# Kernel optimization log

Measured on AMD Instinct MI355X. Metric: run time of the kernel, lower is better.

Reference implementation:

```python
import jax, jax.numpy as jnp
import numpy as np

B, L, D, H = 4, 1024, 1024, 16
E = 16384
HD = D // H  # head dim = 64


def setup_inputs() -> dict:
    key = jax.random.key(0)
    k1, k2, k3, k4 = jax.random.split(key, 4)
    x = jax.random.normal(k1, (B, L, D), dtype=jnp.float32)
    edges = jax.random.randint(k2, (E, 2), 0, L, dtype=jnp.int32)
    w_qkv = jax.random.normal(k3, (3 * D, D), dtype=jnp.float32) * 0.02
    b_qkv = jnp.zeros((3 * D,), dtype=jnp.float32)
    w_out = jax.random.normal(k4, (D, D), dtype=jnp.float32) * 0.02
    b_out = jnp.zeros((D,), dtype=jnp.float32)
    return {"x": x, "edges": edges, "w_qkv": w_qkv, "b_qkv": b_qkv,
            "w_out": w_out, "b_out": b_out}


def reference(x, edges, w_qkv, b_qkv, w_out, b_out):
    # Build symmetric boolean adjacency mask [L, L]; True = edge present.
    adj = jnp.zeros((L, L), dtype=bool)
    adj = adj.at[edges[:, 0], edges[:, 1]].set(True)
    adj = adj.at[edges[:, 1], edges[:, 0]].set(True)

    # Fused QKV projection (torch MultiheadAttention in_proj).
    qkv = x @ w_qkv.T + b_qkv                      # [B, L, 3D]
    q, k, v = jnp.split(qkv, 3, axis=-1)           # each [B, L, D]

    def heads(t):  # [B, L, D] -> [B, H, L, HD]
        return t.reshape(B, L, H, HD).transpose(0, 2, 1, 3)

    q, k, v = heads(q), heads(k), heads(v)
    scale = 1.0 / np.sqrt(HD)
    scores = jnp.einsum('bhqd,bhkd->bhqk', q * scale, k)  # [B, H, L, L]
    # torch bool attn_mask: True means NOT allowed to attend -> -inf.
    scores = jnp.where(adj[None, None, :, :], -jnp.inf, scores)
    attn = jax.nn.softmax(scores, axis=-1)
    out = jnp.einsum('bhqk,bhkd->bhqd', attn, v)   # [B, H, L, HD]
    out = out.transpose(0, 2, 1, 3).reshape(B, L, D)
    return out @ w_out.T + b_out
```

## Files before the change

### kernel.cpp

```cpp
#include <hip/hip_runtime.h>
#include <hip/hip_bf16.h>
#include <stdint.h>

#define B_   4
#define L_   1024
#define D_   1024
#define H_   16
#define HD_  64
#define E_   16384
#define BH_  (B_*H_)
#define BL_  (B_*L_)

typedef __bf16 bf16;
typedef __bf16 bf16x8 __attribute__((ext_vector_type(8)));
typedef float  f32x4  __attribute__((ext_vector_type(4)));

#if __has_builtin(__builtin_amdgcn_exp2f)
#define EXP2F(x) __builtin_amdgcn_exp2f(x)
#else
#define EXP2F(x) exp2f(x)
#endif

#define QSCALE 0.18033688011112042f

__device__ __forceinline__ void gload_lds16(const bf16* gsrc, bf16* lds_dst) {
  __builtin_amdgcn_global_load_lds(
      (const __attribute__((address_space(1))) unsigned int*)gsrc,
      (__attribute__((address_space(3))) unsigned int*)lds_dst,
      16, 0, 0);
}

__global__ void k_detect(const unsigned short* __restrict__ w,
                         unsigned int* __restrict__ flag) {
  int i = blockIdx.x * 256 + threadIdx.x;
  unsigned short u = w[i];
  int e = (u >> 7) & 0xFF;
  if (e >= 200) atomicOr(flag, 1u);
}

__global__ __launch_bounds__(256) void k_castall(
    const void* __restrict__ x, const void* __restrict__ wq,
    const void* __restrict__ wo, const void* __restrict__ bq,
    const void* __restrict__ bo,
    bf16* __restrict__ xb, bf16* __restrict__ wqb, bf16* __restrict__ wob,
    float* __restrict__ bqf, float* __restrict__ bof,
    const unsigned int* __restrict__ flag) {
  const long e = ((long)blockIdx.x * 256 + threadIdx.x) * 8;
  const bool f = *flag != 0;
  const long N0 = 4l << 20, N1 = N0 + (3l << 20), N2 = N1 + (1l << 20);
  const void* src;
  bf16* d16 = nullptr; float* d32 = nullptr; long j;
  if (e < N0)      { src = x;  d16 = xb;  j = e; }
  else if (e < N1) { src = wq; d16 = wqb; j = e - N0; }
  else if (e < N2) { src = wo; d16 = wob; j = e - N1; }
  else {
    long b = e - N2;
    if (b < 3072)      { src = bq; d32 = bqf; j = b; }
    else if (b < 4096) { src = bo; d32 = bof; j = b - 3072; }
    else return;
  }
  if (d16) {
    bf16x8 v;
    if (f) {
      const float* s = (const float*)src + j;
#pragma unroll
      for (int q = 0; q < 8; ++q) v[q] = (bf16)s[q];
    } else {
      v = *(const bf16x8*)((const bf16*)src + j);
    }
    *(bf16x8*)(d16 + j) = v;
  } else {
    if (f) {
      const f32x4* s = (const f32x4*)((const float*)src + j);
      f32x4 a = s[0], b2 = s[1];
      *(f32x4*)(d32 + j) = a;
      *((f32x4*)(d32 + j) + 1) = b2;
    } else {
      const bf16* s = (const bf16*)src + j;
#pragma unroll
      for (int q = 0; q < 8; ++q) d32[j + q] = (float)s[q];
    }
  }
}

__global__ void k_adj(const int* __restrict__ edges,
                      unsigned long long* __restrict__ adj) {
  int i = blockIdx.x * 256 + threadIdx.x;
  if (i < E_) {
    int a = edges[2 * i], b = edges[2 * i + 1];
    atomicOr(&adj[a * 16 + (b >> 6)], 1ull << (b & 63));
    atomicOr(&adj[b * 16 + (a >> 6)], 1ull << (a & 63));
  }
}

template <bool QKV>
__global__ __launch_bounds__(256) void k_gemm(
    const bf16* __restrict__ A, const bf16* __restrict__ W,
    const float* __restrict__ bias, void* __restrict__ outv,
    const unsigned int* __restrict__ flag,
    bf16* __restrict__ qb, bf16* __restrict__ kb, bf16* __restrict__ vb) {
  constexpr int K = 1024;
  __shared__ __align__(16) bf16 As[128 * 32];
  __shared__ __align__(16) bf16 Bs[128 * 32];

  const int t = threadIdx.x;
  const int lane = t & 63, w = t >> 6;
  const int wm = w >> 1, wn = w & 1;
  const int quad = lane >> 4, l16 = lane & 15;
  const int m0 = blockIdx.y * 128, n0 = blockIdx.x * 128;

  const bf16* Abase = A + m0 * K;
  const bf16* Wbase = W + n0 * K;

  f32x4 acc[4][4] = {};

  for (int kt = 0; kt < K; kt += 32) {
#pragma unroll
    for (int j = 0; j < 2; ++j) {
      int o = (j * 256 + t) * 16;
      int row = o >> 6;
      int col = (o & 63) >> 1;
      gload_lds16(Abase + row * K + kt + col, &As[(j * 256 + w * 64) * 8]);
      gload_lds16(Wbase + row * K + kt + col, &Bs[(j * 256 + w * 64) * 8]);
    }
    asm volatile("s_waitcnt vmcnt(0)" ::: "memory");
    __syncthreads();

    bf16x8 af[4], bfv[4];
#pragma unroll
    for (int i = 0; i < 4; ++i) {
      af[i]  = *(const bf16x8*)&As[(wm * 64 + i * 16 + l16) * 32 + quad * 8];
      bfv[i] = *(const bf16x8*)&Bs[(wn * 64 + i * 16 + l16) * 32 + quad * 8];
    }
#pragma unroll
    for (int mi = 0; mi < 4; ++mi)
#pragma unroll
      for (int ni = 0; ni < 4; ++ni)
        acc[mi][ni] = __builtin_amdgcn_mfma_f32_16x16x32_bf16(
            af[mi], bfv[ni], acc[mi][ni], 0, 0, 0);
    __syncthreads();
  }

#pragma unroll
  for (int ni = 0; ni < 4; ++ni) {
    int col = n0 + wn * 64 + ni * 16 + l16;
    float bv = bias[col];
    if constexpr (QKV) {
      int which = col >> 10;
      int hcol = col & 1023;
      int h = hcol >> 6, hd = hcol & 63;
#pragma unroll
      for (int mi = 0; mi < 4; ++mi)
#pragma unroll
        for (int r = 0; r < 4; ++r) {
          int row = m0 + wm * 64 + mi * 16 + quad * 4 + r;
          int bb = row >> 10, l = row & 1023;
          int bh = bb * H_ + h;
          float v = acc[mi][ni][r] + bv;
          if (which == 0)      qb[(bh * L_ + l) * HD_ + hd] = (bf16)(v * QSCALE);
      else if (which == 1)     kb[(bh * L_ + l) * HD_ + hd] = (bf16)v;
      else                     vb[(bh * HD_ + hd) * L_ + l] = (bf16)v;
        }
    } else {
      bool f32out = (*flag != 0);
#pragma unroll
      for (int mi = 0; mi < 4; ++mi)
#pragma unroll
        for (int r = 0; r < 4; ++r) {
          int row = m0 + wm * 64 + mi * 16 + quad * 4 + r;
          float v = acc[mi][ni][r] + bv;
          if (f32out) ((float*)outv)[row * 1024 + col] = v;
          else        ((bf16*)outv)[row * 1024 + col] = (bf16)v;
        }
    }
  }
}

__global__ __launch_bounds__(256, 4) void k_attn(
    const bf16* __restrict__ qb, const bf16* __restrict__ kb,
    const bf16* __restrict__ vb, const unsigned long long* __restrict__ adj,
    bf16* __restrict__ aout) {
  __shared__ __align__(16) bf16 Ks[2 * 64 * 64];
  __shared__ __align__(16) bf16 Vt[2 * 64 * 64];
  __shared__ __align__(16) bf16 Ps[64 * 64];

  const int t = threadIdx.x, lane = t & 63, w = t >> 6;
  const int quad = lane >> 4, l16 = lane & 15;
  const int bh = blockIdx.y, qt = blockIdx.x;
  const int q0 = qt * 64 + w * 16;

  const bf16* qbase = qb + (size_t)bh * (L_ * HD_);
  const bf16* kbase = kb + (size_t)bh * (L_ * HD_);
  const bf16* vbase = vb + (size_t)bh * (HD_ * L_);

  bf16x8 aq[2];
#pragma unroll
  for (int c = 0; c < 2; ++c)
    aq[c] = *(const bf16x8*)&qbase[(q0 + l16) * HD_ + c * 32 + quad * 8];

  const int vr = lane >> 3;
  const int scol = ((lane & 7) ^ vr) * 8;
  const bf16* ksrc0 = kbase + (w * 16 + vr) * HD_ + scol;
  const bf16* ksrc1 = kbase + (w * 16 + 8 + vr) * HD_ + scol;
  const bf16* vsrc0 = vbase + (w * 16 + vr) * L_ + scol;
  const bf16* vsrc1 = vbase + (w * 16 + 8 + vr) * L_ + scol;

  const unsigned long long* adjrow = adj + (size_t)(q0 + quad * 4) * 16;

  float l_acc[4] = {0.f, 0.f, 0.f, 0.f};
  f32x4 o_acc[4] = {};

  const int psoff = (quad * 16) ^ ((l16 & 7) << 4);
  const int pswrow = (w * 16 + quad * 4) * 64;

#define STAGE_KV(i1) do {                                          \
    const int bo_ = ((i1) & 1) * 4096;                             \
    gload_lds16(ksrc0 + (i1) * 4096, &Ks[bo_ + (w * 16) * 64]);     \
    gload_lds16(ksrc1 + (i1) * 4096, &Ks[bo_ + (w * 16 + 8) * 64]); \
    gload_lds16(vsrc0 + (i1) * 64,   &Vt[bo_ + (w * 16) * 64]);     \
    gload_lds16(vsrc1 + (i1) * 64,   &Vt[bo_ + (w * 16 + 8) * 64]); \
  } while (0)

  STAGE_KV(0);

#pragma unroll 1
  for (int i = 0; i < 16; ++i) {
    const int bufo = (i & 1) * 4096;

    unsigned long long wmask[4];
#pragma unroll
    for (int r = 0; r < 4; ++r) wmask[r] = adjrow[r * 16 + i];

    if (i < 15) STAGE_KV(i + 1);

    if (i < 15) asm volatile("s_waitcnt vmcnt(8)" ::: "memory");
    else        asm volatile("s_waitcnt vmcnt(4)" ::: "memory");
    __builtin_amdgcn_s_barrier();

    f32x4 s[4];
#pragma unroll
    for (int nt = 0; nt < 4; ++nt) {
      f32x4 z = {};
#pragma unroll
      for (int c = 0; c < 2; ++c) {
        bf16x8 bk = *(const bf16x8*)&Ks[bufo + (nt * 16 + l16) * 64 +
            ((psoff ^ (c << 6)) >> 1)];
        z = __builtin_amdgcn_mfma_f32_16x16x32_bf16(aq[c], bk, z, 0, 0, 0);
      }
      s[nt] = z;
    }

#pragma unroll
    for (int r = 0; r < 4; ++r) {
      unsigned long long wr = wmask[r] >> l16;
      float pr = 0.f;
#pragma unroll
      for (int nt = 0; nt < 4; ++nt) {
        float sv = s[nt][r];
        if ((wr >> (nt * 16)) & 1ull) sv = -60000.f;
        float p = EXP2F(sv);
        int colb = (nt * 32 + l16 * 2) ^ (((quad * 4 + r) & 7) << 4);
        Ps[pswrow + r * 64 + (colb >> 1)] = (bf16)p;
        pr += p;
      }
      l_acc[r] += pr;
    }

#pragma unroll
    for (int c = 0; c < 2; ++c) {
      bf16x8 ap = *(const bf16x8*)
          &Ps[(w * 16 + l16) * 64 + ((psoff ^ (c << 6)) >> 1)];
#pragma unroll
      for (int nt = 0; nt < 4; ++nt) {
        bf16x8 bv = *(const bf16x8*)
            &Vt[bufo + (nt * 16 + l16) * 64 + ((psoff ^ (c << 6)) >> 1)];
        o_acc[nt] = __builtin_amdgcn_mfma_f32_16x16x32_bf16(ap, bv, o_acc[nt], 0, 0, 0);
      }
    }
    __builtin_amdgcn_s_barrier();
  }
#undef STAGE_KV

#pragma unroll
  for (int x = 1; x < 16; x <<= 1)
#pragma unroll
    for (int r = 0; r < 4; ++r)
      l_acc[r] += __shfl_xor(l_acc[r], x, 64);

  const int bb = bh >> 4, h = bh & 15;
#pragma unroll
  for (int r = 0; r < 4; ++r) {
    const float inv = l_acc[r] > 0.f ? 1.f / l_acc[r] : 0.f;
    const int qrow = q0 + quad * 4 + r;
    bf16* orow = aout + ((size_t)(bb * L_ + qrow)) * D_ + h * HD_;
#pragma unroll
    for (int nt = 0; nt < 4; ++nt)
      orow[nt * 16 + l16] = (bf16)(o_acc[nt][r] * inv);
  }
}

extern "C" void kernel_launch(void* const* d_in, const int* in_sizes, int n_in,
                              void* d_out, int out_size, void* d_ws, size_t ws_size,
                              hipStream_t stream) {
  const void* x_raw  = d_in[0];
  const int*  edges  = (const int*)d_in[1];
  const void* wq_raw = d_in[2];
  const void* bq_raw = d_in[3];
  const void* wo_raw = d_in[4];
  const void* bo_raw = d_in[5];

  char* ws = (char*)d_ws;
  unsigned int*        flag = (unsigned int*)ws;
  unsigned long long*  adj  = (unsigned long long*)(ws + 1024);
  size_t off = 1024 + 131072;
  bf16* xb    = (bf16*)(ws + off); off += (size_t)BL_ * D_ * 2;
  bf16* wqkvb = (bf16*)(ws + off); off += (size_t)3 * D_ * D_ * 2;
  bf16* woutb = (bf16*)(ws + off); off += (size_t)D_ * D_ * 2;
  float* bqf  = (float*)(ws + off); off += 3 * D_ * 4;
  float* bof  = (float*)(ws + off); off += D_ * 4;
  bf16* qb    = (bf16*)(ws + off); off += (size_t)BH_ * L_ * HD_ * 2;
  bf16* kb    = (bf16*)(ws + off); off += (size_t)BH_ * L_ * HD_ * 2;
  bf16* vb    = (bf16*)(ws + off); off += (size_t)BH_ * L_ * HD_ * 2;
  bf16* abuf  = (bf16*)(ws + off);

  hipMemsetAsync(ws, 0, 1024 + 131072, stream);
  k_detect<<<dim3(512), dim3(256), 0, stream>>>(
      (const unsigned short*)wq_raw, flag);

  k_castall<<<dim3(4098), dim3(256), 0, stream>>>(
      x_raw, wq_raw, wo_raw, bq_raw, bo_raw,
      xb, wqkvb, woutb, bqf, bof, flag);

  k_adj<<<dim3(E_ / 256), dim3(256), 0, stream>>>(edges, adj);

  k_gemm<true><<<dim3(24, 32), dim3(256), 0, stream>>>(
      xb, wqkvb, bqf, nullptr, flag, qb, kb, vb);
  k_attn<<<dim3(16, 64), dim3(256), 0, stream>>>(qb, kb, vb, adj, abuf);
  k_gemm<false><<<dim3(8, 32), dim3(256), 0, stream>>>(
      abuf, woutb, bof, d_out, flag, nullptr, nullptr, nullptr);
}
```

Before: 217.1 us.

## Double-buffer GEMM LDS loads with XOR swizzle and fuse detect/adjacency into cast

The GEMM main loop now keeps two LDS buffers and issues the next K-tile's global-to-LDS loads before computing the current one, waiting with a partial vmcnt. This overlaps memory latency with MFMA work. LDS columns are XOR-swizzled by row to reduce bank conflicts on fragment reads. The dtype-detection and adjacency-building kernels are folded into the cast kernel, which removes two launches. Each block now rereads a small slice of the weight to decide the dtype locally, and the LDS footprint doubles.

```diff
diff --git a/kernel.cpp b/kernel.cpp
--- a/kernel.cpp
+++ b/kernel.cpp
@@ -14,6 +14,7 @@
 typedef __bf16 bf16;
 typedef __bf16 bf16x8 __attribute__((ext_vector_type(8)));
 typedef float  f32x4  __attribute__((ext_vector_type(4)));
+typedef unsigned short u16x8 __attribute__((ext_vector_type(8)));
 
 #if __has_builtin(__builtin_amdgcn_exp2f)
 #define EXP2F(x) __builtin_amdgcn_exp2f(x)
@@ -30,23 +31,33 @@
       16, 0, 0);
 }
 
-__global__ void k_detect(const unsigned short* __restrict__ w,
-                         unsigned int* __restrict__ flag) {
-  int i = blockIdx.x * 256 + threadIdx.x;
-  unsigned short u = w[i];
-  int e = (u >> 7) & 0xFF;
-  if (e >= 200) atomicOr(flag, 1u);
-}
-
 __global__ __launch_bounds__(256) void k_castall(
     const void* __restrict__ x, const void* __restrict__ wq,
     const void* __restrict__ wo, const void* __restrict__ bq,
     const void* __restrict__ bo,
+    const int* __restrict__ edges, unsigned long long* __restrict__ adj,
     bf16* __restrict__ xb, bf16* __restrict__ wqb, bf16* __restrict__ wob,
     float* __restrict__ bqf, float* __restrict__ bof,
-    const unsigned int* __restrict__ flag) {
-  const long e = ((long)blockIdx.x * 256 + threadIdx.x) * 8;
-  const bool f = *flag != 0;
+    unsigned int* __restrict__ flag_out) {
+  const int t = threadIdx.x;
+
+  bool lf = false;
+  {
+    u16x8 u = *(const u16x8*)((const unsigned short*)wq + (size_t)t * 8);
+#pragma unroll
+    for (int q = 0; q < 8; ++q) lf |= (((u[q] >> 7) & 0xFF) >= 200);
+  }
+  const bool f = __any(lf);
+  if (blockIdx.x == 0 && t == 0 && f) *flag_out = 1u;
+
+  if (blockIdx.x < 64) {
+    int i = blockIdx.x * 256 + t;
+    int a = edges[2 * i], b = edges[2 * i + 1];
+    atomicOr(&adj[a * 16 + (b >> 6)], 1ull << (b & 63));
+    atomicOr(&adj[b * 16 + (a >> 6)], 1ull << (a & 63));
+  }
+
+  const long e = ((long)blockIdx.x * 256 + t) * 8;
   const long N0 = 4l << 20, N1 = N0 + (3l << 20), N2 = N1 + (1l << 20);
   const void* src;
   bf16* d16 = nullptr; float* d32 = nullptr; long j;
@@ -83,16 +94,6 @@
   }
 }
 
-__global__ void k_adj(const int* __restrict__ edges,
-                      unsigned long long* __restrict__ adj) {
-  int i = blockIdx.x * 256 + threadIdx.x;
-  if (i < E_) {
-    int a = edges[2 * i], b = edges[2 * i + 1];
-    atomicOr(&adj[a * 16 + (b >> 6)], 1ull << (b & 63));
-    atomicOr(&adj[b * 16 + (a >> 6)], 1ull << (a & 63));
-  }
-}
-
 template <bool QKV>
 __global__ __launch_bounds__(256) void k_gemm(
     const bf16* __restrict__ A, const bf16* __restrict__ W,
@@ -100,8 +101,8 @@
     const unsigned int* __restrict__ flag,
     bf16* __restrict__ qb, bf16* __restrict__ kb, bf16* __restrict__ vb) {
   constexpr int K = 1024;
-  __shared__ __align__(16) bf16 As[128 * 32];
-  __shared__ __align__(16) bf16 Bs[128 * 32];
+  __shared__ __align__(16) bf16 As[2 * 128 * 32];
+  __shared__ __align__(16) bf16 Bs[2 * 128 * 32];
 
   const int t = threadIdx.x;
   const int lane = t & 63, w = t >> 6;
@@ -112,25 +113,43 @@
   const bf16* Abase = A + m0 * K;
   const bf16* Wbase = W + n0 * K;
 
+  const int srow = t >> 2;
+  const int scolb = (t & 3) << 4;
+  const int scol = (scolb ^ ((srow & 3) << 4)) >> 1;
+  const bf16* asrc0 = Abase + srow * K + scol;
+  const bf16* asrc1 = Abase + (srow + 64) * K + scol;
+  const bf16* wsrc0 = Wbase + srow * K + scol;
+  const bf16* wsrc1 = Wbase + (srow + 64) * K + scol;
+
+  const int fo = ((quad * 16) ^ ((l16 & 3) << 4)) >> 1;
+
   f32x4 acc[4][4] = {};
 
-  for (int kt = 0; kt < K; kt += 32) {
-#pragma unroll
-    for (int j = 0; j < 2; ++j) {
-      int o = (j * 256 + t) * 16;
-      int row = o >> 6;
-      int col = (o & 63) >> 1;
-      gload_lds16(Abase + row * K + kt + col, &As[(j * 256 + w * 64) * 8]);
-      gload_lds16(Wbase + row * K + kt + col, &Bs[(j * 256 + w * 64) * 8]);
-    }
-    asm volatile("s_waitcnt vmcnt(0)" ::: "memory");
-    __syncthreads();
+#define STAGE_AB(it1) do {                                          \
+    const int bo_ = ((it1) & 1) * 4096;                              \
+    gload_lds16(asrc0 + (it1) * 32, &As[bo_ + (w * 64) * 8]);        \
+    gload_lds16(asrc1 + (it1) * 32, &As[bo_ + (256 + w * 64) * 8]);  \
+    gload_lds16(wsrc0 + (it1) * 32, &Bs[bo_ + (w * 64) * 8]);        \
+    gload_lds16(wsrc1 + (it1) * 32, &Bs[bo_ + (256 + w * 64) * 8]);  \
+  } while (0)
+
+  STAGE_AB(0);
+
+#pragma unroll 1
+  for (int it = 0; it < 32; ++it) {
+    const int bo = (it & 1) * 4096;
+
+    if (it < 31) STAGE_AB(it + 1);
+
+    if (it < 31) asm volatile("s_waitcnt vmcnt(4)" ::: "memory");
+    else         asm volatile("s_waitcnt vmcnt(0)" ::: "memory");
+    __builtin_amdgcn_s_barrier();
 
     bf16x8 af[4], bfv[4];
 #pragma unroll
     for (int i = 0; i < 4; ++i) {
-      af[i]  = *(const bf16x8*)&As[(wm * 64 + i * 16 + l16) * 32 + quad * 8];
-      bfv[i] = *(const bf16x8*)&Bs[(wn * 64 + i * 16 + l16) * 32 + quad * 8];
+      af[i]  = *(const bf16x8*)&As[bo + (wm * 64 + i * 16 + l16) * 32 + fo];
+      bfv[i] = *(const bf16x8*)&Bs[bo + (wn * 64 + i * 16 + l16) * 32 + fo];
     }
 #pragma unroll
     for (int mi = 0; mi < 4; ++mi)
@@ -138,8 +157,9 @@
       for (int ni = 0; ni < 4; ++ni)
         acc[mi][ni] = __builtin_amdgcn_mfma_f32_16x16x32_bf16(
             af[mi], bfv[ni], acc[mi][ni], 0, 0, 0);
-    __syncthreads();
-  }
+    __builtin_amdgcn_s_barrier();
+  }
+#undef STAGE_AB
 
 #pragma unroll
   for (int ni = 0; ni < 4; ++ni) {
@@ -324,14 +344,10 @@
   bf16* abuf  = (bf16*)(ws + off);
 
   hipMemsetAsync(ws, 0, 1024 + 131072, stream);
-  k_detect<<<dim3(512), dim3(256), 0, stream>>>(
-      (const unsigned short*)wq_raw, flag);
 
   k_castall<<<dim3(4098), dim3(256), 0, stream>>>(
-      x_raw, wq_raw, wo_raw, bq_raw, bo_raw,
+      x_raw, wq_raw, wo_raw, bq_raw, bo_raw, edges, adj,
       xb, wqkvb, woutb, bqf, bof, flag);
-
-  k_adj<<<dim3(E_ / 256), dim3(256), 0, stream>>>(edges, adj);
 
   k_gemm<true><<<dim3(24, 32), dim3(256), 0, stream>>>(
       xb, wqkvb, bqf, nullptr, flag, qb, kb, vb);
```

Measured after the change: 190.3 us. 1.14x faster.
